# Kernel tuning notes

Hardware: AMD Instinct MI355X
Metric: run time of the kernel (lower is better)

Reference implementation:

```python
import jax, jax.numpy as jnp
import numpy as np

N_NODES = 100000
N_EDGES = 1600000
N_GRAPHS = 1000


def _gcn_layer(x, W, b, row, col, dinv):
    # GCNConv with improved=True: A_hat = A + 2I, symmetric normalization.
    xw = x @ W  # [N, out]
    norm = dinv[row] * dinv[col]  # [E]
    agg = jax.ops.segment_sum(norm[:, None] * xw[row], col, num_segments=N_NODES)
    # self-loop contribution with fill weight 2.0
    agg = agg + (2.0 * dinv * dinv)[:, None] * xw
    return agg + b


def setup_inputs() -> dict:
    key = jax.random.key(0)
    ks = jax.random.split(key, 20)
    x = jax.random.normal(ks[0], (N_NODES, 336), dtype=jnp.float32)
    edge_index = jax.random.randint(ks[1], (2, N_EDGES), 0, N_NODES, dtype=jnp.int64)
    batch = jnp.sort(jax.random.randint(ks[2], (N_NODES,), 0, N_GRAPHS, dtype=jnp.int64))
    def lin(k, din, dout):
        s = 1.0 / np.sqrt(din)
        return jax.random.uniform(k, (din, dout), jnp.float32, -s, s)
    params = {
        'W1': lin(ks[3], 336, 100), 'b1': jnp.zeros((100,), jnp.float32),
        'W2': lin(ks[4], 100, 100), 'b2': jnp.zeros((100,), jnp.float32),
        'W3': lin(ks[5], 100, 100), 'b3': jnp.zeros((100,), jnp.float32),
        'W4': lin(ks[6], 100, 100), 'b4': jnp.zeros((100,), jnp.float32),
        'W5': lin(ks[7], 100, 100), 'b5': jnp.zeros((100,), jnp.float32),
        'Wl1': lin(ks[8], 100, 100), 'bl1': jnp.zeros((100,), jnp.float32),
        'Wl2': lin(ks[9], 100, 100), 'bl2': jnp.zeros((100,), jnp.float32),
        'Wl3': lin(ks[10], 100, 29), 'bl3': jnp.zeros((29,), jnp.float32),
    }
    return {'x': x, 'edge_index': edge_index, 'batch': batch, **params}


def reference(x, edge_index, batch, W1, b1, W2, b2, W3, b3, W4, b4, W5, b5,
              Wl1, bl1, Wl2, bl2, Wl3, bl3):
    row, col = edge_index[0], edge_index[1]
    # degree of A + 2I (edge weights are 1, self-loop weight 2)
    deg = jax.ops.segment_sum(jnp.ones((N_EDGES,), x.dtype), col, num_segments=N_NODES) + 2.0
    dinv = deg ** -0.5
    h = jax.nn.relu(_gcn_layer(x, W1, b1, row, col, dinv))
    h = jax.nn.relu(_gcn_layer(h, W2, b2, row, col, dinv))
    h = jax.nn.relu(_gcn_layer(h, W3, b3, row, col, dinv))
    h = jax.nn.relu(_gcn_layer(h, W4, b4, row, col, dinv))
    h = jax.nn.relu(_gcn_layer(h, W5, b5, row, col, dinv))
    # global mean pool over graphs
    sums = jax.ops.segment_sum(h, batch, num_segments=N_GRAPHS)
    counts = jax.ops.segment_sum(jnp.ones((N_NODES,), h.dtype), batch, num_segments=N_GRAPHS)
    pooled = sums / jnp.maximum(counts, 1.0)[:, None]
    g = jax.nn.relu(pooled @ Wl1 + bl1)
    g = jax.nn.relu(g @ Wl2 + bl2)
    return g @ Wl3 + bl3
```

## Files before the change

kernel.cpp:

```cpp
#include <hip/hip_runtime.h>
#include <hip/hip_fp16.h>
#include <stdint.h>

#define NN 100000
#define NE 1600000
#define NG 1000
#define LDA 112
#define LDX 128

typedef float f32x4 __attribute__((ext_vector_type(4)));
typedef _Float16 f16x8 __attribute__((ext_vector_type(8)));

__device__ __forceinline__ void load_lds16(const void* g, void* l) {
    __builtin_amdgcn_global_load_lds((const __attribute__((address_space(1))) unsigned int*)g,
                                     (__attribute__((address_space(3))) unsigned int*)l,
                                     16, 0, 0);
}

__global__ void k_deg(const int* __restrict__ col, int* __restrict__ degcnt) {
    int e = blockIdx.x * 256 + threadIdx.x;
    if (e < NE) atomicAdd(&degcnt[col[e]], 1);
}

__global__ void k_scan1(const int* __restrict__ cnt, int* __restrict__ csum) {
    __shared__ int s[256];
    int i = blockIdx.x * 256 + threadIdx.x;
    s[threadIdx.x] = (i < NN) ? cnt[i] : 0;
    __syncthreads();
    for (int o = 128; o > 0; o >>= 1) {
        if (threadIdx.x < o) s[threadIdx.x] += s[threadIdx.x + o];
        __syncthreads();
    }
    if (threadIdx.x == 0) csum[blockIdx.x] = s[0];
}

__global__ void k_scan2(const int* __restrict__ csum, int* __restrict__ csum2, int nb) {
    __shared__ int s[512];
    int t = threadIdx.x;
    int v = (t < nb) ? csum[t] : 0;
    s[t] = v; __syncthreads();
    for (int o = 1; o < 512; o <<= 1) {
        int x = (t >= o) ? s[t - o] : 0;
        __syncthreads();
        s[t] += x;
        __syncthreads();
    }
    if (t < nb) csum2[t] = s[t] - v;
}

__global__ void k_scan3d(const int* __restrict__ cnt, const int* __restrict__ csum2,
                         int* __restrict__ indptr, float* __restrict__ dinv) {
    __shared__ int s[256];
    int t = threadIdx.x;
    int i = blockIdx.x * 256 + t;
    int v = (i < NN) ? cnt[i] : 0;
    s[t] = v; __syncthreads();
    for (int o = 1; o < 256; o <<= 1) {
        int x = (t >= o) ? s[t - o] : 0;
        __syncthreads();
        s[t] += x;
        __syncthreads();
    }
    if (i < NN) {
        indptr[i] = csum2[blockIdx.x] + s[t] - v;
        dinv[i] = 1.0f / sqrtf((float)v + 2.0f);
    }
    if (i == 0) indptr[NN] = NE;
}

__global__ void k_scatter(const int* __restrict__ row, const int* __restrict__ col,
                          const int* __restrict__ indptr,
                          int* __restrict__ fill, int* __restrict__ esrc) {
    int e = blockIdx.x * 256 + threadIdx.x;
    if (e >= NE) return;
    int r = row[e], c = col[e];
    int pos = indptr[c] + atomicAdd(&fill[c], 1);
    esrc[pos] = r;
}

__global__ void k_gbounds(const int* __restrict__ batch, int* __restrict__ gstart) {
    int i = blockIdx.x * 256 + threadIdx.x;
    if (i >= NN) return;
    int b = batch[i];
    int pb = (i == 0) ? -1 : batch[i - 1];
    for (int g = pb + 1; g <= b; g++) gstart[g] = i;
    if (i == NN - 1) {
        for (int g = b + 1; g <= NG; g++) gstart[g] = NN;
    }
}

__global__ void k_convW(const float* __restrict__ W1, __half* __restrict__ w1h, __half* __restrict__ w1l,
                        const float* __restrict__ W2, __half* __restrict__ w2h, __half* __restrict__ w2l,
                        const float* __restrict__ W3, __half* __restrict__ w3h, __half* __restrict__ w3l,
                        const float* __restrict__ W4, __half* __restrict__ w4h, __half* __restrict__ w4l,
                        const float* __restrict__ W5, __half* __restrict__ w5h, __half* __restrict__ w5l) {
    int b = blockIdx.x, t = threadIdx.x;
    const float* W; __half *Wh, *Wl; int K, KCP, idx;
    if (b < 168) {
        W = W1; Wh = w1h; Wl = w1l; K = 336; KCP = 384; idx = b * 256 + t;
    } else {
        int li = (b - 168) / 56;
        int lb = (b - 168) % 56;
        const float* Ws[4] = {W2, W3, W4, W5};
        __half* Whs[4] = {w2h, w3h, w4h, w5h};
        __half* Wls[4] = {w2l, w3l, w4l, w5l};
        W = Ws[li]; Wh = Whs[li]; Wl = Wls[li]; K = 100; KCP = 128; idx = lb * 256 + t;
    }
    int n = idx / KCP, k = idx - n * KCP;
    float v = (n < 100 && k < K) ? W[k * 100 + n] : 0.f;
    __half hi = __float2half(v);
    Wh[idx] = hi;
    Wl[idx] = __float2half((v - __half2float(hi)) * 2048.f);
}

__global__ __launch_bounds__(256) void k_gemmX(const float* __restrict__ x,
                                               const __half* __restrict__ Whi,
                                               const __half* __restrict__ Wlo,
                                               const float* __restrict__ dinv,
                                               __half* __restrict__ out) {
    __shared__ __align__(16) __half Ah[64 * 128];
    __shared__ __align__(16) __half Hs[112 * 128];
    __shared__ __align__(16) __half Ls[112 * 128];
    int t = threadIdx.x;
    int lane = t & 63, wv = t >> 6;
    int l15 = lane & 15, quad = lane >> 4;
    int rowbase = blockIdx.x * 64;

    f32x4 acch[7], accl[7];
#pragma unroll
    for (int i = 0; i < 7; i++)
#pragma unroll
        for (int r = 0; r < 4; r++) { acch[i][r] = 0.f; accl[i][r] = 0.f; }

    for (int k0 = 0; k0 < 384; k0 += 128) {
        __syncthreads();
#pragma unroll
        for (int j = 0; j < 7; j++) {
            int o = (t + j * 256) * 16;
            int r = o >> 8;
            int scb = (o & 255) ^ ((r & 7) << 4);
            size_t goff = (size_t)r * 768 + (size_t)k0 * 2 + scb;
            load_lds16((const char*)Whi + goff, (char*)Hs + o);
            load_lds16((const char*)Wlo + goff, (char*)Ls + o);
        }
#pragma unroll
        for (int j = 0; j < 4; j++) {
            int i = t + j * 256;
            int r = i >> 4;
            int o = i * 16;
            int sc = (o & 255) ^ ((r & 7) << 4);
            int rowg = rowbase + r;
            int k = k0 + (sc >> 1);
            float4 v0 = make_float4(0.f, 0.f, 0.f, 0.f), v1 = v0;
            if (rowg < NN && k < 336) {
                const float* p = x + (size_t)rowg * 336 + k;
                v0 = *(const float4*)p;
                v1 = *(const float4*)(p + 4);
            }
            __half2 p0 = __floats2half2_rn(v0.x, v0.y);
            __half2 p1 = __floats2half2_rn(v0.z, v0.w);
            __half2 p2 = __floats2half2_rn(v1.x, v1.y);
            __half2 p3 = __floats2half2_rn(v1.z, v1.w);
            uint4 pk;
            pk.x = __builtin_bit_cast(unsigned, p0);
            pk.y = __builtin_bit_cast(unsigned, p1);
            pk.z = __builtin_bit_cast(unsigned, p2);
            pk.w = __builtin_bit_cast(unsigned, p3);
            *(uint4*)((char*)Ah + o) = pk;
        }
        __syncthreads();
        int swz = (l15 & 7) << 4;
        const char* abase = (const char*)Ah + (wv * 16 + l15) * 256;
#pragma unroll
        for (int ks = 0; ks < 4; ks++) {
            int cb = (ks * 64 + quad * 16) ^ swz;
            f16x8 a = *(const f16x8*)(abase + cb);
#pragma unroll
            for (int tt = 0; tt < 7; tt++) {
                int nrow = tt * 16 + l15;
                f16x8 bh = *(const f16x8*)((const char*)Hs + nrow * 256 + cb);
                f16x8 bl = *(const f16x8*)((const char*)Ls + nrow * 256 + cb);
                acch[tt] = __builtin_amdgcn_mfma_f32_16x16x32_f16(a, bh, acch[tt], 0, 0, 0);
                accl[tt] = __builtin_amdgcn_mfma_f32_16x16x32_f16(a, bl, accl[tt], 0, 0, 0);
            }
        }
    }

    int gr0 = rowbase + wv * 16 + quad * 4;
    float dv[4];
#pragma unroll
    for (int reg = 0; reg < 4; reg++) dv[reg] = (gr0 + reg < NN) ? dinv[gr0 + reg] : 0.f;
#pragma unroll
    for (int tt = 0; tt < 7; tt++) {
        int n = tt * 16 + l15;
#pragma unroll
        for (int reg = 0; reg < 4; reg++) {
            int gr = gr0 + reg;
            if (gr < NN)
                out[(size_t)gr * LDX + n] =
                    __float2half(dv[reg] * (acch[tt][reg] + accl[tt][reg] * (1.f / 2048.f)));
        }
    }
    if (l15 < 8) {
#pragma unroll
        for (int reg = 0; reg < 4; reg++) {
            int gr = gr0 + reg;
            if (gr < NN) *(unsigned int*)(out + (size_t)gr * LDX + 112 + l15 * 2) = 0u;
        }
    }
}

__global__ __launch_bounds__(256) void k_gemmH(const __half* __restrict__ act,
                                               const __half* __restrict__ Whi,
                                               const __half* __restrict__ Wlo,
                                               const float* __restrict__ dinv,
                                               __half* __restrict__ out) {
    __shared__ __align__(16) __half Ah[64 * 128];
    __shared__ __align__(16) __half Hs[112 * 128];
    __shared__ __align__(16) __half Ls[112 * 128];
    int t = threadIdx.x;
    int lane = t & 63, wv = t >> 6;
    int l15 = lane & 15, quad = lane >> 4;
    int rowbase = blockIdx.x * 64;

#pragma unroll
    for (int j = 0; j < 4; j++) {
        int o = (t + j * 256) * 16;
        int r = o >> 8;
        int scb = (o & 255) ^ ((r & 7) << 4);
        load_lds16((const char*)act + (size_t)(rowbase + r) * 256 + scb, (char*)Ah + o);
    }
#pragma unroll
    for (int j = 0; j < 7; j++) {
        int o = (t + j * 256) * 16;
        int r = o >> 8;
        int scb = (o & 255) ^ ((r & 7) << 4);
        size_t goff = (size_t)r * 256 + scb;
        load_lds16((const char*)Whi + goff, (char*)Hs + o);
        load_lds16((const char*)Wlo + goff, (char*)Ls + o);
    }

    f32x4 acch[7], accl[7];
#pragma unroll
    for (int i = 0; i < 7; i++)
#pragma unroll
        for (int r = 0; r < 4; r++) { acch[i][r] = 0.f; accl[i][r] = 0.f; }

    __syncthreads();
    int swz = (l15 & 7) << 4;
    const char* abase = (const char*)Ah + (wv * 16 + l15) * 256;
#pragma unroll
    for (int ks = 0; ks < 4; ks++) {
        int cb = (ks * 64 + quad * 16) ^ swz;
        f16x8 a = *(const f16x8*)(abase + cb);
#pragma unroll
        for (int tt = 0; tt < 7; tt++) {
            int nrow = tt * 16 + l15;
            f16x8 bh = *(const f16x8*)((const char*)Hs + nrow * 256 + cb);
            f16x8 bl = *(const f16x8*)((const char*)Ls + nrow * 256 + cb);
            acch[tt] = __builtin_amdgcn_mfma_f32_16x16x32_f16(a, bh, acch[tt], 0, 0, 0);
            accl[tt] = __builtin_amdgcn_mfma_f32_16x16x32_f16(a, bl, accl[tt], 0, 0, 0);
        }
    }

    int gr0 = rowbase + wv * 16 + quad * 4;
    float dv[4];
#pragma unroll
    for (int reg = 0; reg < 4; reg++) dv[reg] = (gr0 + reg < NN) ? dinv[gr0 + reg] : 0.f;
#pragma unroll
    for (int tt = 0; tt < 7; tt++) {
        int n = tt * 16 + l15;
#pragma unroll
        for (int reg = 0; reg < 4; reg++) {
            int gr = gr0 + reg;
            if (gr < NN)
                out[(size_t)gr * LDX + n] =
                    __float2half(dv[reg] * (acch[tt][reg] + accl[tt][reg] * (1.f / 2048.f)));
        }
    }
    if (l15 < 8) {
#pragma unroll
        for (int reg = 0; reg < 4; reg++) {
            int gr = gr0 + reg;
            if (gr < NN) *(unsigned int*)(out + (size_t)gr * LDX + 112 + l15 * 2) = 0u;
        }
    }
}

__device__ __forceinline__ void agg_core(const __half* __restrict__ xs,
                                         const int* __restrict__ esrc,
                                         int beg, int end, int lane, int col,
                                         float& ax, float& ay) {
    ax = 0.f; ay = 0.f;
    for (int c = beg; c < end; c += 64) {
        int m = min(64, end - c);
        int se = 0;
        if (lane < m) se = esrc[c + lane];
        int j = 0;
        for (; j + 16 <= m; j += 16) {
            __half2 v[16];
#pragma unroll
            for (int u = 0; u < 16; u++) {
                int s = __builtin_amdgcn_readlane(se, j + u);
                v[u] = *(const __half2*)(xs + (size_t)s * LDX + col);
            }
#pragma unroll
            for (int u = 0; u < 16; u++) {
                float2 f = __half22float2(v[u]);
                ax += f.x; ay += f.y;
            }
        }
        for (; j + 8 <= m; j += 8) {
            __half2 v[8];
#pragma unroll
            for (int u = 0; u < 8; u++) {
                int s = __builtin_amdgcn_readlane(se, j + u);
                v[u] = *(const __half2*)(xs + (size_t)s * LDX + col);
            }
#pragma unroll
            for (int u = 0; u < 8; u++) {
                float2 f = __half22float2(v[u]);
                ax += f.x; ay += f.y;
            }
        }
        for (; j + 4 <= m; j += 4) {
            __half2 v[4];
#pragma unroll
            for (int u = 0; u < 4; u++) {
                int s = __builtin_amdgcn_readlane(se, j + u);
                v[u] = *(const __half2*)(xs + (size_t)s * LDX + col);
            }
#pragma unroll
            for (int u = 0; u < 4; u++) {
                float2 f = __half22float2(v[u]);
                ax += f.x; ay += f.y;
            }
        }
        for (; j < m; j++) {
            int s = __builtin_amdgcn_readlane(se, j);
            float2 f = __half22float2(*(const __half2*)(xs + (size_t)s * LDX + col));
            ax += f.x; ay += f.y;
        }
    }
}

__global__ __launch_bounds__(256) void k_aggS(const __half* __restrict__ xs,
                                              const int* __restrict__ indptr,
                                              const int* __restrict__ esrc,
                                              const float* __restrict__ dinv,
                                              const float* __restrict__ bias,
                                              __half* __restrict__ hh) {
    int wave = threadIdx.x >> 6;
    int lane = threadIdx.x & 63;
    int n = blockIdx.x * 4 + wave;
    if (n >= NN) return;
    int beg = indptr[n], end = indptr[n + 1];
    int col = (lane < 50) ? lane * 2 : 0;
    float ax, ay;
    agg_core(xs, esrc, beg, end, lane, col, ax, ay);
    if (lane < 50) {
        float di = dinv[n];
        float2 xv = __half22float2(*(const __half2*)(xs + (size_t)n * LDX + col));
        float2 bv = *(const float2*)(bias + lane * 2);
        float hx = fmaxf(di * (ax + 2.f * xv.x) + bv.x, 0.f);
        float hy = fmaxf(di * (ay + 2.f * xv.y) + bv.y, 0.f);
        *(__half2*)(hh + (size_t)n * LDX + col) = __floats2half2_rn(hx, hy);
    } else {
        int pc = 100 + (lane - 50) * 2;
        *(unsigned int*)(hh + (size_t)n * LDX + pc) = 0u;
    }
}

__global__ __launch_bounds__(256) void k_agg(const __half* __restrict__ xs,
                                             const int* __restrict__ indptr,
                                             const int* __restrict__ esrc,
                                             const float* __restrict__ dinv,
                                             const float* __restrict__ bias,
                                             float* __restrict__ hout) {
    int wave = threadIdx.x >> 6;
    int lane = threadIdx.x & 63;
    int n = blockIdx.x * 4 + wave;
    if (n >= NN) return;
    int beg = indptr[n], end = indptr[n + 1];
    int col = (lane < 50) ? lane * 2 : 0;
    float ax, ay;
    agg_core(xs, esrc, beg, end, lane, col, ax, ay);
    if (lane < 50) {
        float di = dinv[n];
        float2 xv = __half22float2(*(const __half2*)(xs + (size_t)n * LDX + col));
        float2 bv = *(const float2*)(bias + lane * 2);
        float2 r;
        r.x = fmaxf(di * (ax + 2.f * xv.x) + bv.x, 0.f);
        r.y = fmaxf(di * (ay + 2.f * xv.y) + bv.y, 0.f);
        *(float2*)(hout + (size_t)n * LDA + col) = r;
    }
}

__global__ __launch_bounds__(128) void k_pool(const float* __restrict__ h,
                                              const int* __restrict__ gstart,
                                              float* __restrict__ pooled) {
    int g = blockIdx.x, t = threadIdx.x;
    if (t >= 100) return;
    int st = gstart[g];
    int cnt = gstart[g + 1] - st;
    float s0 = 0.f, s1 = 0.f, s2 = 0.f, s3 = 0.f;
    float s4 = 0.f, s5 = 0.f, s6 = 0.f, s7 = 0.f;
    int i = 0;
    for (; i + 8 <= cnt; i += 8) {
        s0 += h[(size_t)(st + i) * LDA + t];
        s1 += h[(size_t)(st + i + 1) * LDA + t];
        s2 += h[(size_t)(st + i + 2) * LDA + t];
        s3 += h[(size_t)(st + i + 3) * LDA + t];
        s4 += h[(size_t)(st + i + 4) * LDA + t];
        s5 += h[(size_t)(st + i + 5) * LDA + t];
        s6 += h[(size_t)(st + i + 6) * LDA + t];
        s7 += h[(size_t)(st + i + 7) * LDA + t];
    }
    for (; i < cnt; i++) s0 += h[(size_t)(st + i) * LDA + t];
    float s = ((s0 + s1) + (s2 + s3)) + ((s4 + s5) + (s6 + s7));
    pooled[g * 100 + t] = s / (float)(cnt > 0 ? cnt : 1);
}

__global__ void k_mlp(const float* __restrict__ pooled,
                      const float* __restrict__ Wl1, const float* __restrict__ bl1,
                      const float* __restrict__ Wl2, const float* __restrict__ bl2,
                      const float* __restrict__ Wl3, const float* __restrict__ bl3,
                      float* __restrict__ out) {
    __shared__ float p[100], q[100];
    int g = blockIdx.x, t = threadIdx.x;
    if (t < 100) p[t] = pooled[g * 100 + t];
    __syncthreads();
    float s1 = 0.f;
    if (t < 100) {
        s1 = bl1[t];
        for (int k = 0; k < 100; k++) s1 += p[k] * Wl1[k * 100 + t];
        s1 = fmaxf(s1, 0.f);
    }
    __syncthreads();
    if (t < 100) q[t] = s1;
    __syncthreads();
    float s2 = 0.f;
    if (t < 100) {
        s2 = bl2[t];
        for (int k = 0; k < 100; k++) s2 += q[k] * Wl2[k * 100 + t];
        s2 = fmaxf(s2, 0.f);
    }
    __syncthreads();
    if (t < 100) p[t] = s2;
    __syncthreads();
    if (t < 29) {
        float s3 = bl3[t];
        for (int k = 0; k < 100; k++) s3 += p[k] * Wl3[k * 29 + t];
        out[g * 29 + t] = s3;
    }
}

extern "C" void kernel_launch(void* const* d_in, const int* in_sizes, int n_in,
                              void* d_out, int out_size, void* d_ws, size_t ws_size,
                              hipStream_t stream) {
    const float* x     = (const float*)d_in[0];
    const int*   ei    = (const int*)d_in[1];
    const int*   batch = (const int*)d_in[2];
    const float* W1 = (const float*)d_in[3];  const float* b1 = (const float*)d_in[4];
    const float* W2 = (const float*)d_in[5];  const float* b2 = (const float*)d_in[6];
    const float* W3 = (const float*)d_in[7];  const float* b3 = (const float*)d_in[8];
    const float* W4 = (const float*)d_in[9];  const float* b4 = (const float*)d_in[10];
    const float* W5 = (const float*)d_in[11]; const float* b5 = (const float*)d_in[12];
    const float* Wl1 = (const float*)d_in[13]; const float* bl1 = (const float*)d_in[14];
    const float* Wl2 = (const float*)d_in[15]; const float* bl2 = (const float*)d_in[16];
    const float* Wl3 = (const float*)d_in[17]; const float* bl3 = (const float*)d_in[18];
    float* out = (float*)d_out;

    const int* row = ei;
    const int* col = ei + NE;

    uintptr_t base = (uintptr_t)d_ws;
    auto alloc = [&](size_t bytes) -> void* {
        void* p = (void*)base;
        base += (bytes + 255) & ~(size_t)255;
        return p;
    };
    int*   cnts   = (int*)alloc((size_t)(2 * NN) * 4);
    int*   degcnt = cnts;
    int*   fill   = cnts + NN;
    float* dinv   = (float*)alloc(NN * 4);
    int*   indptr = (int*)alloc((NN + 1) * 4);
    int*   csum   = (int*)alloc(512 * 4);
    int*   csum2  = (int*)alloc(512 * 4);
    int*   gstart = (int*)alloc((NG + 1) * 4);
    int*   esrc   = (int*)alloc((size_t)NE * 4);
    __half* xsh   = (__half*)alloc((size_t)NN * LDX * 2 + 8192);
    __half* hh    = (__half*)alloc((size_t)NN * LDX * 2 + 8192);
    float* h      = (float*)alloc((size_t)NN * LDA * 4);
    float* pooled = (float*)alloc((size_t)NG * 100 * 4);
    __half* w1hi = (__half*)alloc((size_t)112 * 384 * 2);
    __half* w1lo = (__half*)alloc((size_t)112 * 384 * 2);
    __half* w2hi = (__half*)alloc((size_t)112 * 128 * 2);
    __half* w2lo = (__half*)alloc((size_t)112 * 128 * 2);
    __half* w3hi = (__half*)alloc((size_t)112 * 128 * 2);
    __half* w3lo = (__half*)alloc((size_t)112 * 128 * 2);
    __half* w4hi = (__half*)alloc((size_t)112 * 128 * 2);
    __half* w4lo = (__half*)alloc((size_t)112 * 128 * 2);
    __half* w5hi = (__half*)alloc((size_t)112 * 128 * 2);
    __half* w5lo = (__half*)alloc((size_t)112 * 128 * 2);

    hipMemsetAsync(cnts, 0, (size_t)(2 * NN) * 4, stream);

    const int NB = (NN + 255) / 256;
    k_deg<<<(NE + 255) / 256, 256, 0, stream>>>(col, degcnt);
    k_scan1<<<NB, 256, 0, stream>>>(degcnt, csum);
    k_scan2<<<1, 512, 0, stream>>>(csum, csum2, NB);
    k_scan3d<<<NB, 256, 0, stream>>>(degcnt, csum2, indptr, dinv);
    k_scatter<<<(NE + 255) / 256, 256, 0, stream>>>(row, col, indptr, fill, esrc);
    k_gbounds<<<NB, 256, 0, stream>>>(batch, gstart);
    k_convW<<<392, 256, 0, stream>>>(W1, w1hi, w1lo, W2, w2hi, w2lo,
                                     W3, w3hi, w3lo, W4, w4hi, w4lo,
                                     W5, w5hi, w5lo);

    const int GEMM_GRID = (NN + 63) / 64;
    const int AGG_GRID = (NN + 3) / 4;

    k_gemmX<<<GEMM_GRID, 256, 0, stream>>>(x, w1hi, w1lo, dinv, xsh);
    k_aggS<<<AGG_GRID, 256, 0, stream>>>(xsh, indptr, esrc, dinv, b1, hh);
    k_gemmH<<<GEMM_GRID, 256, 0, stream>>>(hh, w2hi, w2lo, dinv, xsh);
    k_aggS<<<AGG_GRID, 256, 0, stream>>>(xsh, indptr, esrc, dinv, b2, hh);
    k_gemmH<<<GEMM_GRID, 256, 0, stream>>>(hh, w3hi, w3lo, dinv, xsh);
    k_aggS<<<AGG_GRID, 256, 0, stream>>>(xsh, indptr, esrc, dinv, b3, hh);
    k_gemmH<<<GEMM_GRID, 256, 0, stream>>>(hh, w4hi, w4lo, dinv, xsh);
    k_aggS<<<AGG_GRID, 256, 0, stream>>>(xsh, indptr, esrc, dinv, b4, hh);
    k_gemmH<<<GEMM_GRID, 256, 0, stream>>>(hh, w5hi, w5lo, dinv, xsh);
    k_agg<<<AGG_GRID, 256, 0, stream>>>(xsh, indptr, esrc, dinv, b5, h);

    k_pool<<<NG, 128, 0, stream>>>(h, gstart, pooled);
    k_mlp<<<NG, 128, 0, stream>>>(pooled, Wl1, bl1, Wl2, bl2, Wl3, bl3, out);
}
```

Before: 908.6 us.

## Drop LDS staging in GEMMs and load MFMA operands directly from global memory

Both dense GEMM kernels now skip shared memory. Each wave loads its A fragments and the split-fp16 weight fragments straight from global memory into registers, and each wave covers 32 rows instead of 16, so a block handles 128 rows. This removes the LDS fills, barriers and swizzle arithmetic and allows more blocks per CU (launch bounds 256,3). In exchange the weight fragments are re-read from global or cache by every wave, and the fp32 x loads in the first layer are uncoalesced 32-byte segments per lane.

```diff
diff --git a/kernel.cpp b/kernel.cpp
--- a/kernel.cpp
+++ b/kernel.cpp
@@ -10,12 +10,6 @@
 
 typedef float f32x4 __attribute__((ext_vector_type(4)));
 typedef _Float16 f16x8 __attribute__((ext_vector_type(8)));
-
-__device__ __forceinline__ void load_lds16(const void* g, void* l) {
-    __builtin_amdgcn_global_load_lds((const __attribute__((address_space(1))) unsigned int*)g,
-                                     (__attribute__((address_space(3))) unsigned int*)l,
-                                     16, 0, 0);
-}
 
 __global__ void k_deg(const int* __restrict__ col, int* __restrict__ degcnt) {
     int e = blockIdx.x * 256 + threadIdx.x;
@@ -113,176 +107,157 @@
     Wl[idx] = __float2half((v - __half2float(hi)) * 2048.f);
 }
 
-__global__ __launch_bounds__(256) void k_gemmX(const float* __restrict__ x,
-                                               const __half* __restrict__ Whi,
-                                               const __half* __restrict__ Wlo,
-                                               const float* __restrict__ dinv,
-                                               __half* __restrict__ out) {
-    __shared__ __align__(16) __half Ah[64 * 128];
-    __shared__ __align__(16) __half Hs[112 * 128];
-    __shared__ __align__(16) __half Ls[112 * 128];
+__device__ __forceinline__ f16x8 cvt8(float4 v0, float4 v1) {
+    __half2 p0 = __floats2half2_rn(v0.x, v0.y);
+    __half2 p1 = __floats2half2_rn(v0.z, v0.w);
+    __half2 p2 = __floats2half2_rn(v1.x, v1.y);
+    __half2 p3 = __floats2half2_rn(v1.z, v1.w);
+    union { uint4 u; f16x8 f; } c;
+    c.u.x = __builtin_bit_cast(unsigned, p0);
+    c.u.y = __builtin_bit_cast(unsigned, p1);
+    c.u.z = __builtin_bit_cast(unsigned, p2);
+    c.u.w = __builtin_bit_cast(unsigned, p3);
+    return c.f;
+}
+
+__device__ __forceinline__ f16x8 load_cvt(const float* __restrict__ x, int row, int k) {
+    float4 v0 = make_float4(0.f, 0.f, 0.f, 0.f), v1 = v0;
+    if (row < NN && k < 336) {
+        const float* p = x + (size_t)row * 336 + k;
+        v0 = *(const float4*)p;
+        v1 = *(const float4*)(p + 4);
+    }
+    return cvt8(v0, v1);
+}
+
+__global__ __launch_bounds__(256, 3) void k_gemmX(const float* __restrict__ x,
+                                                  const __half* __restrict__ Whi,
+                                                  const __half* __restrict__ Wlo,
+                                                  const float* __restrict__ dinv,
+                                                  __half* __restrict__ out) {
     int t = threadIdx.x;
     int lane = t & 63, wv = t >> 6;
     int l15 = lane & 15, quad = lane >> 4;
-    int rowbase = blockIdx.x * 64;
-
-    f32x4 acch[7], accl[7];
-#pragma unroll
-    for (int i = 0; i < 7; i++)
-#pragma unroll
-        for (int r = 0; r < 4; r++) { acch[i][r] = 0.f; accl[i][r] = 0.f; }
-
-    for (int k0 = 0; k0 < 384; k0 += 128) {
-        __syncthreads();
-#pragma unroll
-        for (int j = 0; j < 7; j++) {
-            int o = (t + j * 256) * 16;
-            int r = o >> 8;
-            int scb = (o & 255) ^ ((r & 7) << 4);
-            size_t goff = (size_t)r * 768 + (size_t)k0 * 2 + scb;
-            load_lds16((const char*)Whi + goff, (char*)Hs + o);
-            load_lds16((const char*)Wlo + goff, (char*)Ls + o);
-        }
-#pragma unroll
-        for (int j = 0; j < 4; j++) {
-            int i = t + j * 256;
-            int r = i >> 4;
-            int o = i * 16;
-            int sc = (o & 255) ^ ((r & 7) << 4);
-            int rowg = rowbase + r;
-            int k = k0 + (sc >> 1);
-            float4 v0 = make_float4(0.f, 0.f, 0.f, 0.f), v1 = v0;
-            if (rowg < NN && k < 336) {
-                const float* p = x + (size_t)rowg * 336 + k;
-                v0 = *(const float4*)p;
-                v1 = *(const float4*)(p + 4);
-            }
-            __half2 p0 = __floats2half2_rn(v0.x, v0.y);
-            __half2 p1 = __floats2half2_rn(v0.z, v0.w);
-            __half2 p2 = __floats2half2_rn(v1.x, v1.y);
-            __half2 p3 = __floats2half2_rn(v1.z, v1.w);
-            uint4 pk;
-            pk.x = __builtin_bit_cast(unsigned, p0);
-            pk.y = __builtin_bit_cast(unsigned, p1);
-            pk.z = __builtin_bit_cast(unsigned, p2);
-            pk.w = __builtin_bit_cast(unsigned, p3);
-            *(uint4*)((char*)Ah + o) = pk;
-        }
-        __syncthreads();
-        int swz = (l15 & 7) << 4;
-        const char* abase = (const char*)Ah + (wv * 16 + l15) * 256;
-#pragma unroll
-        for (int ks = 0; ks < 4; ks++) {
-            int cb = (ks * 64 + quad * 16) ^ swz;
-            f16x8 a = *(const f16x8*)(abase + cb);
-#pragma unroll
-            for (int tt = 0; tt < 7; tt++) {
-                int nrow = tt * 16 + l15;
-                f16x8 bh = *(const f16x8*)((const char*)Hs + nrow * 256 + cb);
-                f16x8 bl = *(const f16x8*)((const char*)Ls + nrow * 256 + cb);
-                acch[tt] = __builtin_amdgcn_mfma_f32_16x16x32_f16(a, bh, acch[tt], 0, 0, 0);
-                accl[tt] = __builtin_amdgcn_mfma_f32_16x16x32_f16(a, bl, accl[tt], 0, 0, 0);
-            }
-        }
-    }
-
-    int gr0 = rowbase + wv * 16 + quad * 4;
-    float dv[4];
-#pragma unroll
-    for (int reg = 0; reg < 4; reg++) dv[reg] = (gr0 + reg < NN) ? dinv[gr0 + reg] : 0.f;
-#pragma unroll
-    for (int tt = 0; tt < 7; tt++) {
-        int n = tt * 16 + l15;
-#pragma unroll
-        for (int reg = 0; reg < 4; reg++) {
-            int gr = gr0 + reg;
-            if (gr < NN)
-                out[(size_t)gr * LDX + n] =
-                    __float2half(dv[reg] * (acch[tt][reg] + accl[tt][reg] * (1.f / 2048.f)));
-        }
-    }
-    if (l15 < 8) {
-#pragma unroll
-        for (int reg = 0; reg < 4; reg++) {
-            int gr = gr0 + reg;
-            if (gr < NN) *(unsigned int*)(out + (size_t)gr * LDX + 112 + l15 * 2) = 0u;
-        }
-    }
-}
-
-__global__ __launch_bounds__(256) void k_gemmH(const __half* __restrict__ act,
-                                               const __half* __restrict__ Whi,
-                                               const __half* __restrict__ Wlo,
-                                               const float* __restrict__ dinv,
-                                               __half* __restrict__ out) {
-    __shared__ __align__(16) __half Ah[64 * 128];
-    __shared__ __align__(16) __half Hs[112 * 128];
-    __shared__ __align__(16) __half Ls[112 * 128];
+    int rowbase = blockIdx.x * 128 + wv * 32;
+
+    f32x4 acch[2][7], accl[2][7];
+#pragma unroll
+    for (int rg = 0; rg < 2; rg++)
+#pragma unroll
+        for (int i = 0; i < 7; i++)
+#pragma unroll
+            for (int r = 0; r < 4; r++) { acch[rg][i][r] = 0.f; accl[rg][i][r] = 0.f; }
+
+    int ar0 = rowbase + l15;
+    const __half* bh0 = Whi + (size_t)l15 * 384 + quad * 8;
+    const __half* bl0 = Wlo + (size_t)l15 * 384 + quad * 8;
+
+#pragma unroll
+    for (int ks = 0; ks < 11; ks++) {
+        int k = ks * 32 + quad * 8;
+        f16x8 a0 = load_cvt(x, ar0, k);
+        f16x8 a1 = load_cvt(x, ar0 + 16, k);
+#pragma unroll
+        for (int tt = 0; tt < 7; tt++) {
+            f16x8 bh = *(const f16x8*)(bh0 + (size_t)tt * 16 * 384 + ks * 32);
+            f16x8 bl = *(const f16x8*)(bl0 + (size_t)tt * 16 * 384 + ks * 32);
+            acch[0][tt] = __builtin_amdgcn_mfma_f32_16x16x32_f16(a0, bh, acch[0][tt], 0, 0, 0);
+            accl[0][tt] = __builtin_amdgcn_mfma_f32_16x16x32_f16(a0, bl, accl[0][tt], 0, 0, 0);
+            acch[1][tt] = __builtin_amdgcn_mfma_f32_16x16x32_f16(a1, bh, acch[1][tt], 0, 0, 0);
+            accl[1][tt] = __builtin_amdgcn_mfma_f32_16x16x32_f16(a1, bl, accl[1][tt], 0, 0, 0);
+        }
+    }
+
+#pragma unroll
+    for (int rg = 0; rg < 2; rg++) {
+        int gr0 = rowbase + rg * 16 + quad * 4;
+        float dv[4];
+#pragma unroll
+        for (int reg = 0; reg < 4; reg++) dv[reg] = (gr0 + reg < NN) ? dinv[gr0 + reg] : 0.f;
+#pragma unroll
+        for (int tt = 0; tt < 7; tt++) {
+            int n = tt * 16 + l15;
+#pragma unroll
+            for (int reg = 0; reg < 4; reg++) {
+                int gr = gr0 + reg;
+                if (gr < NN)
+                    out[(size_t)gr * LDX + n] =
+                        __float2half(dv[reg] * (acch[rg][tt][reg] + accl[rg][tt][reg] * (1.f / 2048.f)));
+            }
+        }
+        if (l15 < 8) {
+#pragma unroll
+            for (int reg = 0; reg < 4; reg++) {
+                int gr = gr0 + reg;
+                if (gr < NN) *(unsigned int*)(out + (size_t)gr * LDX + 112 + l15 * 2) = 0u;
+            }
+        }
+    }
+}
+
+__global__ __launch_bounds__(256, 3) void k_gemmH(const __half* __restrict__ act,
+                                                  const __half* __restrict__ Whi,
+                                                  const __half* __restrict__ Wlo,
+                                                  const float* __restrict__ dinv,
+                                                  __half* __restrict__ out) {
     int t = threadIdx.x;
     int lane = t & 63, wv = t >> 6;
     int l15 = lane & 15, quad = lane >> 4;
-    int rowbase = blockIdx.x * 64;
-
-#pragma unroll
-    for (int j = 0; j < 4; j++) {
-        int o = (t + j * 256) * 16;
-        int r = o >> 8;
-        int scb = (o & 255) ^ ((r & 7) << 4);
-        load_lds16((const char*)act + (size_t)(rowbase + r) * 256 + scb, (char*)Ah + o);
-    }
-#pragma unroll
-    for (int j = 0; j < 7; j++) {
-        int o = (t + j * 256) * 16;
-        int r = o >> 8;
-        int scb = (o & 255) ^ ((r & 7) << 4);
-        size_t goff = (size_t)r * 256 + scb;
-        load_lds16((const char*)Whi + goff, (char*)Hs + o);
-        load_lds16((const char*)Wlo + goff, (char*)Ls + o);
-    }
-
-    f32x4 acch[7], accl[7];
-#pragma unroll
-    for (int i = 0; i < 7; i++)
-#pragma unroll
-        for (int r = 0; r < 4; r++) { acch[i][r] = 0.f; accl[i][r] = 0.f; }
-
-    __syncthreads();
-    int swz = (l15 & 7) << 4;
-    const char* abase = (const char*)Ah + (wv * 16 + l15) * 256;
+    int rowbase = blockIdx.x * 128 + wv * 32;
+
+    f32x4 acch[2][7], accl[2][7];
+#pragma unroll
+    for (int rg = 0; rg < 2; rg++)
+#pragma unroll
+        for (int i = 0; i < 7; i++)
+#pragma unroll
+            for (int r = 0; r < 4; r++) { acch[rg][i][r] = 0.f; accl[rg][i][r] = 0.f; }
+
+    int r0 = min(rowbase + l15, NN - 1);
+    int r1 = min(rowbase + l15 + 16, NN - 1);
+    const __half* a0p = act + (size_t)r0 * LDX + quad * 8;
+    const __half* a1p = act + (size_t)r1 * LDX + quad * 8;
+    const __half* bh0 = Whi + (size_t)l15 * 128 + quad * 8;
+    const __half* bl0 = Wlo + (size_t)l15 * 128 + quad * 8;
+
 #pragma unroll
     for (int ks = 0; ks < 4; ks++) {
-        int cb = (ks * 64 + quad * 16) ^ swz;
-        f16x8 a = *(const f16x8*)(abase + cb);
+        f16x8 a0 = *(const f16x8*)(a0p + ks * 32);
+        f16x8 a1 = *(const f16x8*)(a1p + ks * 32);
 #pragma unroll
         for (int tt = 0; tt < 7; tt++) {
-            int nrow = tt * 16 + l15;
-            f16x8 bh = *(const f16x8*)((const char*)Hs + nrow * 256 + cb);
-            f16x8 bl = *(const f16x8*)((const char*)Ls + nrow * 256 + cb);
-            acch[tt] = __builtin_amdgcn_mfma_f32_16x16x32_f16(a, bh, acch[tt], 0, 0, 0);
-            accl[tt] = __builtin_amdgcn_mfma_f32_16x16x32_f16(a, bl, accl[tt], 0, 0, 0);
-        }
-    }
-
-    int gr0 = rowbase + wv * 16 + quad * 4;
-    float dv[4];
-#pragma unroll
-    for (int reg = 0; reg < 4; reg++) dv[reg] = (gr0 + reg < NN) ? dinv[gr0 + reg] : 0.f;
-#pragma unroll
-    for (int tt = 0; tt < 7; tt++) {
-        int n = tt * 16 + l15;
-#pragma unroll
-        for (int reg = 0; reg < 4; reg++) {
-            int gr = gr0 + reg;
-            if (gr < NN)
-                out[(size_t)gr * LDX + n] =
-                    __float2half(dv[reg] * (acch[tt][reg] + accl[tt][reg] * (1.f / 2048.f)));
-        }
-    }
-    if (l15 < 8) {
-#pragma unroll
-        for (int reg = 0; reg < 4; reg++) {
-            int gr = gr0 + reg;
-            if (gr < NN) *(unsigned int*)(out + (size_t)gr * LDX + 112 + l15 * 2) = 0u;
+            f16x8 bh = *(const f16x8*)(bh0 + (size_t)tt * 16 * 128 + ks * 32);
+            f16x8 bl = *(const f16x8*)(bl0 + (size_t)tt * 16 * 128 + ks * 32);
+            acch[0][tt] = __builtin_amdgcn_mfma_f32_16x16x32_f16(a0, bh, acch[0][tt], 0, 0, 0);
+            accl[0][tt] = __builtin_amdgcn_mfma_f32_16x16x32_f16(a0, bl, accl[0][tt], 0, 0, 0);
+            acch[1][tt] = __builtin_amdgcn_mfma_f32_16x16x32_f16(a1, bh, acch[1][tt], 0, 0, 0);
+            accl[1][tt] = __builtin_amdgcn_mfma_f32_16x16x32_f16(a1, bl, accl[1][tt], 0, 0, 0);
+        }
+    }
+
+#pragma unroll
+    for (int rg = 0; rg < 2; rg++) {
+        int gr0 = rowbase + rg * 16 + quad * 4;
+        float dv[4];
+#pragma unroll
+        for (int reg = 0; reg < 4; reg++) dv[reg] = (gr0 + reg < NN) ? dinv[gr0 + reg] : 0.f;
+#pragma unroll
+        for (int tt = 0; tt < 7; tt++) {
+            int n = tt * 16 + l15;
+#pragma unroll
+            for (int reg = 0; reg < 4; reg++) {
+                int gr = gr0 + reg;
+                if (gr < NN)
+                    out[(size_t)gr * LDX + n] =
+                        __float2half(dv[reg] * (acch[rg][tt][reg] + accl[rg][tt][reg] * (1.f / 2048.f)));
+            }
+        }
+        if (l15 < 8) {
+#pragma unroll
+            for (int reg = 0; reg < 4; reg++) {
+                int gr = gr0 + reg;
+                if (gr < NN) *(unsigned int*)(out + (size_t)gr * LDX + 112 + l15 * 2) = 0u;
+            }
         }
     }
 }
@@ -489,8 +464,8 @@
     int*   csum2  = (int*)alloc(512 * 4);
     int*   gstart = (int*)alloc((NG + 1) * 4);
     int*   esrc   = (int*)alloc((size_t)NE * 4);
-    __half* xsh   = (__half*)alloc((size_t)NN * LDX * 2 + 8192);
-    __half* hh    = (__half*)alloc((size_t)NN * LDX * 2 + 8192);
+    __half* xsh   = (__half*)alloc((size_t)NN * LDX * 2);
+    __half* hh    = (__half*)alloc((size_t)NN * LDX * 2);
     float* h      = (float*)alloc((size_t)NN * LDA * 4);
     float* pooled = (float*)alloc((size_t)NG * 100 * 4);
     __half* w1hi = (__half*)alloc((size_t)112 * 384 * 2);
@@ -517,7 +492,7 @@
                                      W3, w3hi, w3lo, W4, w4hi, w4lo,
                                      W5, w5hi, w5lo);
 
-    const int GEMM_GRID = (NN + 63) / 64;
+    const int GEMM_GRID = (NN + 127) / 128;
     const int AGG_GRID = (NN + 3) / 4;
 
     k_gemmX<<<GEMM_GRID, 256, 0, stream>>>(x, w1hi, w1lo, dinv, xsh);
```

After: 1.028 ms. 1.13x slower.

## Load GEMM A operands directly into registers and pre-swizzle weights

Applied to the files above, without the earlier changes.

The GEMM kernels no longer stage the activation tile in LDS. Each lane loads its A fragment straight from global memory into registers, converting to fp16 on the fly for the first layer. Weight hi/lo tensors are stored pre-swizzled by the conversion kernel, so the LDS weight copy becomes a plain linear copy. Blocks grow to 512 threads covering 128 rows, which halves the number of times each block reloads the weights into LDS. The cost is uncoalesced per-lane global reads for A and a larger block size that may limit occupancy.

```diff
diff --git a/kernel.cpp b/kernel.cpp
--- a/kernel.cpp
+++ b/kernel.cpp
@@ -109,22 +109,38 @@
     int n = idx / KCP, k = idx - n * KCP;
     float v = (n < 100 && k < K) ? W[k * 100 + n] : 0.f;
     __half hi = __float2half(v);
-    Wh[idx] = hi;
-    Wl[idx] = __float2half((v - __half2float(hi)) * 2048.f);
-}
-
-__global__ __launch_bounds__(256) void k_gemmX(const float* __restrict__ x,
-                                               const __half* __restrict__ Whi,
-                                               const __half* __restrict__ Wlo,
-                                               const float* __restrict__ dinv,
-                                               __half* __restrict__ out) {
-    __shared__ __align__(16) __half Ah[64 * 128];
+    __half lo = __float2half((v - __half2float(hi)) * 2048.f);
+    int kc = k & 127;
+    size_t so = (size_t)n * KCP + (k - kc) + (kc ^ ((n & 7) << 3));
+    Wh[so] = hi;
+    Wl[so] = lo;
+}
+
+__device__ __forceinline__ f16x8 cvt8(float4 v0, float4 v1) {
+    __half2 p0 = __floats2half2_rn(v0.x, v0.y);
+    __half2 p1 = __floats2half2_rn(v0.z, v0.w);
+    __half2 p2 = __floats2half2_rn(v1.x, v1.y);
+    __half2 p3 = __floats2half2_rn(v1.z, v1.w);
+    union { uint4 u; f16x8 f; } c;
+    c.u.x = __builtin_bit_cast(unsigned, p0);
+    c.u.y = __builtin_bit_cast(unsigned, p1);
+    c.u.z = __builtin_bit_cast(unsigned, p2);
+    c.u.w = __builtin_bit_cast(unsigned, p3);
+    return c.f;
+}
+
+__global__ __launch_bounds__(512, 4) void k_gemmX(const float* __restrict__ x,
+                                                  const __half* __restrict__ Whi,
+                                                  const __half* __restrict__ Wlo,
+                                                  const float* __restrict__ dinv,
+                                                  __half* __restrict__ out) {
     __shared__ __align__(16) __half Hs[112 * 128];
     __shared__ __align__(16) __half Ls[112 * 128];
     int t = threadIdx.x;
     int lane = t & 63, wv = t >> 6;
     int l15 = lane & 15, quad = lane >> 4;
-    int rowbase = blockIdx.x * 64;
+    int rowbase = blockIdx.x * 128;
+    int arow = rowbase + wv * 16 + l15;
 
     f32x4 acch[7], accl[7];
 #pragma unroll
@@ -132,56 +148,43 @@
 #pragma unroll
         for (int r = 0; r < 4; r++) { acch[i][r] = 0.f; accl[i][r] = 0.f; }
 
+    int swz = (l15 & 7) << 4;
+
     for (int k0 = 0; k0 < 384; k0 += 128) {
-        __syncthreads();
-#pragma unroll
-        for (int j = 0; j < 7; j++) {
-            int o = (t + j * 256) * 16;
-            int r = o >> 8;
-            int scb = (o & 255) ^ ((r & 7) << 4);
-            size_t goff = (size_t)r * 768 + (size_t)k0 * 2 + scb;
-            load_lds16((const char*)Whi + goff, (char*)Hs + o);
-            load_lds16((const char*)Wlo + goff, (char*)Ls + o);
-        }
-#pragma unroll
-        for (int j = 0; j < 4; j++) {
-            int i = t + j * 256;
-            int r = i >> 4;
-            int o = i * 16;
-            int sc = (o & 255) ^ ((r & 7) << 4);
-            int rowg = rowbase + r;
-            int k = k0 + (sc >> 1);
+        if (k0) __syncthreads();
+        f16x8 a[4];
+#pragma unroll
+        for (int ks = 0; ks < 4; ks++) {
+            int k = k0 + ks * 32 + quad * 8;
             float4 v0 = make_float4(0.f, 0.f, 0.f, 0.f), v1 = v0;
-            if (rowg < NN && k < 336) {
-                const float* p = x + (size_t)rowg * 336 + k;
+            if (arow < NN && k < 336) {
+                const float* p = x + (size_t)arow * 336 + k;
                 v0 = *(const float4*)p;
                 v1 = *(const float4*)(p + 4);
             }
-            __half2 p0 = __floats2half2_rn(v0.x, v0.y);
-            __half2 p1 = __floats2half2_rn(v0.z, v0.w);
-            __half2 p2 = __floats2half2_rn(v1.x, v1.y);
-            __half2 p3 = __floats2half2_rn(v1.z, v1.w);
-            uint4 pk;
-            pk.x = __builtin_bit_cast(unsigned, p0);
-            pk.y = __builtin_bit_cast(unsigned, p1);
-            pk.z = __builtin_bit_cast(unsigned, p2);
-            pk.w = __builtin_bit_cast(unsigned, p3);
-            *(uint4*)((char*)Ah + o) = pk;
+            a[ks] = cvt8(v0, v1);
+        }
+#pragma unroll
+        for (int cch = 0; cch < 7; cch++) {
+            int g = wv + cch * 8;
+            int tb = (g >= 28);
+            int o = (g - (tb ? 28 : 0)) * 1024 + lane * 16;
+            int r = o >> 8, cc = o & 255;
+            size_t src = (size_t)r * 768 + (size_t)(k0 * 2) + cc;
+            if (!tb) load_lds16((const char*)Whi + src, (char*)Hs + o);
+            else     load_lds16((const char*)Wlo + src, (char*)Ls + o);
         }
         __syncthreads();
-        int swz = (l15 & 7) << 4;
-        const char* abase = (const char*)Ah + (wv * 16 + l15) * 256;
 #pragma unroll
         for (int ks = 0; ks < 4; ks++) {
             int cb = (ks * 64 + quad * 16) ^ swz;
-            f16x8 a = *(const f16x8*)(abase + cb);
 #pragma unroll
             for (int tt = 0; tt < 7; tt++) {
-                int nrow = tt * 16 + l15;
-                f16x8 bh = *(const f16x8*)((const char*)Hs + nrow * 256 + cb);
-                f16x8 bl = *(const f16x8*)((const char*)Ls + nrow * 256 + cb);
-                acch[tt] = __builtin_amdgcn_mfma_f32_16x16x32_f16(a, bh, acch[tt], 0, 0, 0);
-                accl[tt] = __builtin_amdgcn_mfma_f32_16x16x32_f16(a, bl, accl[tt], 0, 0, 0);
+                int ro = (tt * 16 + l15) * 256;
+                f16x8 bh = *(const f16x8*)((const char*)Hs + ro + cb);
+                f16x8 bl = *(const f16x8*)((const char*)Ls + ro + cb);
+                acch[tt] = __builtin_amdgcn_mfma_f32_16x16x32_f16(a[ks], bh, acch[tt], 0, 0, 0);
+                accl[tt] = __builtin_amdgcn_mfma_f32_16x16x32_f16(a[ks], bl, accl[tt], 0, 0, 0);
             }
         }
     }
@@ -210,34 +213,32 @@
     }
 }
 
-__global__ __launch_bounds__(256) void k_gemmH(const __half* __restrict__ act,
-                                               const __half* __restrict__ Whi,
-                                               const __half* __restrict__ Wlo,
-                                               const float* __restrict__ dinv,
-                                               __half* __restrict__ out) {
-    __shared__ __align__(16) __half Ah[64 * 128];
+__global__ __launch_bounds__(512, 4) void k_gemmH(const __half* __restrict__ act,
+                                                  const __half* __restrict__ Whi,
+                                                  const __half* __restrict__ Wlo,
+                                                  const float* __restrict__ dinv,
+                                                  __half* __restrict__ out) {
     __shared__ __align__(16) __half Hs[112 * 128];
     __shared__ __align__(16) __half Ls[112 * 128];
     int t = threadIdx.x;
     int lane = t & 63, wv = t >> 6;
     int l15 = lane & 15, quad = lane >> 4;
-    int rowbase = blockIdx.x * 64;
-
-#pragma unroll
-    for (int j = 0; j < 4; j++) {
-        int o = (t + j * 256) * 16;
-        int r = o >> 8;
-        int scb = (o & 255) ^ ((r & 7) << 4);
-        load_lds16((const char*)act + (size_t)(rowbase + r) * 256 + scb, (char*)Ah + o);
-    }
-#pragma unroll
-    for (int j = 0; j < 7; j++) {
-        int o = (t + j * 256) * 16;
-        int r = o >> 8;
-        int scb = (o & 255) ^ ((r & 7) << 4);
-        size_t goff = (size_t)r * 256 + scb;
-        load_lds16((const char*)Whi + goff, (char*)Hs + o);
-        load_lds16((const char*)Wlo + goff, (char*)Ls + o);
+    int rowbase = blockIdx.x * 128;
+    int ar = min(rowbase + wv * 16 + l15, NN - 1);
+
+    const char* ap = (const char*)act + (size_t)ar * 256;
+    f16x8 a[4];
+#pragma unroll
+    for (int ks = 0; ks < 4; ks++)
+        a[ks] = *(const f16x8*)(ap + ks * 64 + quad * 16);
+
+#pragma unroll
+    for (int cch = 0; cch < 7; cch++) {
+        int g = wv + cch * 8;
+        int tb = (g >= 28);
+        int o = (g - (tb ? 28 : 0)) * 1024 + lane * 16;
+        if (!tb) load_lds16((const char*)Whi + o, (char*)Hs + o);
+        else     load_lds16((const char*)Wlo + o, (char*)Ls + o);
     }
 
     f32x4 acch[7], accl[7];
@@ -248,18 +249,16 @@
 
     __syncthreads();
     int swz = (l15 & 7) << 4;
-    const char* abase = (const char*)Ah + (wv * 16 + l15) * 256;
 #pragma unroll
     for (int ks = 0; ks < 4; ks++) {
         int cb = (ks * 64 + quad * 16) ^ swz;
-        f16x8 a = *(const f16x8*)(abase + cb);
 #pragma unroll
         for (int tt = 0; tt < 7; tt++) {
-            int nrow = tt * 16 + l15;
-            f16x8 bh = *(const f16x8*)((const char*)Hs + nrow * 256 + cb);
-            f16x8 bl = *(const f16x8*)((const char*)Ls + nrow * 256 + cb);
-            acch[tt] = __builtin_amdgcn_mfma_f32_16x16x32_f16(a, bh, acch[tt], 0, 0, 0);
-            accl[tt] = __builtin_amdgcn_mfma_f32_16x16x32_f16(a, bl, accl[tt], 0, 0, 0);
+            int ro = (tt * 16 + l15) * 256;
+            f16x8 bh = *(const f16x8*)((const char*)Hs + ro + cb);
+            f16x8 bl = *(const f16x8*)((const char*)Ls + ro + cb);
+            acch[tt] = __builtin_amdgcn_mfma_f32_16x16x32_f16(a[ks], bh, acch[tt], 0, 0, 0);
+            accl[tt] = __builtin_amdgcn_mfma_f32_16x16x32_f16(a[ks], bl, accl[tt], 0, 0, 0);
         }
     }
 
@@ -489,8 +488,8 @@
     int*   csum2  = (int*)alloc(512 * 4);
     int*   gstart = (int*)alloc((NG + 1) * 4);
     int*   esrc   = (int*)alloc((size_t)NE * 4);
-    __half* xsh   = (__half*)alloc((size_t)NN * LDX * 2 + 8192);
-    __half* hh    = (__half*)alloc((size_t)NN * LDX * 2 + 8192);
+    __half* xsh   = (__half*)alloc((size_t)NN * LDX * 2);
+    __half* hh    = (__half*)alloc((size_t)NN * LDX * 2);
     float* h      = (float*)alloc((size_t)NN * LDA * 4);
     float* pooled = (float*)alloc((size_t)NG * 100 * 4);
     __half* w1hi = (__half*)alloc((size_t)112 * 384 * 2);
@@ -517,18 +516,18 @@
                                      W3, w3hi, w3lo, W4, w4hi, w4lo,
                                      W5, w5hi, w5lo);
 
-    const int GEMM_GRID = (NN + 63) / 64;
+    const int GEMM_GRID = (NN + 127) / 128;
     const int AGG_GRID = (NN + 3) / 4;
 
-    k_gemmX<<<GEMM_GRID, 256, 0, stream>>>(x, w1hi, w1lo, dinv, xsh);
+    k_gemmX<<<GEMM_GRID, 512, 0, stream>>>(x, w1hi, w1lo, dinv, xsh);
     k_aggS<<<AGG_GRID, 256, 0, stream>>>(xsh, indptr, esrc, dinv, b1, hh);
-    k_gemmH<<<GEMM_GRID, 256, 0, stream>>>(hh, w2hi, w2lo, dinv, xsh);
+    k_gemmH<<<GEMM_GRID, 512, 0, stream>>>(hh, w2hi, w2lo, dinv, xsh);
     k_aggS<<<AGG_GRID, 256, 0, stream>>>(xsh, indptr, esrc, dinv, b2, hh);
-    k_gemmH<<<GEMM_GRID, 256, 0, stream>>>(hh, w3hi, w3lo, dinv, xsh);
+    k_gemmH<<<GEMM_GRID, 512, 0, stream>>>(hh, w3hi, w3lo, dinv, xsh);
     k_aggS<<<AGG_GRID, 256, 0, stream>>>(xsh, indptr, esrc, dinv, b3, hh);
-    k_gemmH<<<GEMM_GRID, 256, 0, stream>>>(hh, w4hi, w4lo, dinv, xsh);
+    k_gemmH<<<GEMM_GRID, 512, 0, stream>>>(hh, w4hi, w4lo, dinv, xsh);
     k_aggS<<<AGG_GRID, 256, 0, stream>>>(xsh, indptr, esrc, dinv, b4, hh);
-    k_gemmH<<<GEMM_GRID, 256, 0, stream>>>(hh, w5hi, w5lo, dinv, xsh);
+    k_gemmH<<<GEMM_GRID, 512, 0, stream>>>(hh, w5hi, w5lo, dinv, xsh);
     k_agg<<<AGG_GRID, 256, 0, stream>>>(xsh, indptr, esrc, dinv, b5, h);
 
     k_pool<<<NG, 128, 0, stream>>>(h, gstart, pooled);
```

New measurement: 846.2 us. 1.07x faster.
